# Kernel optimization log

Measured on AMD Instinct MI355X. Metric: run time of the kernel, lower is better.

The kernel has to match this reference:

```python
import jax, jax.numpy as jnp
import numpy as np

N = 2_097_152
EPS = 1e-6


def _tri(x):
    # triangleWave (period 2), maps R -> [0, 1]; applied to 'normalize=True' tables
    return 2.0 * jnp.abs(x / 2.0 - jnp.floor(x / 2.0 + 0.5))


def _grid2d(uv, table, bilinear, normalize):
    # uv: (N,2) in [0,1); table: (U,V,L)
    t = _tri(table) if normalize else table
    U, V, _ = t.shape
    u = jnp.clip(uv[:, 0], 0.0, 1.0 - EPS) * (U - 1)
    v = jnp.clip(uv[:, 1], 0.0, 1.0 - EPS) * (V - 1)
    if bilinear:
        u0 = jnp.floor(u)
        v0 = jnp.floor(v)
        fu = (u - u0)[:, None]
        fv = (v - v0)[:, None]
        u0i = u0.astype(jnp.int32)
        v0i = v0.astype(jnp.int32)
        u1i = jnp.minimum(u0i + 1, U - 1)
        v1i = jnp.minimum(v0i + 1, V - 1)
        return (t[u0i, v0i] * (1 - fu) * (1 - fv)
                + t[u1i, v0i] * fu * (1 - fv)
                + t[u0i, v1i] * (1 - fu) * fv
                + t[u1i, v1i] * fu * fv)
    return t[jnp.round(u).astype(jnp.int32), jnp.round(v).astype(jnp.int32)]


def _grid1d(u, table, bilinear, normalize):
    # u: (N,) in [0,1); table: (U,L)
    t = _tri(table) if normalize else table
    U, _ = t.shape
    uu = jnp.clip(u, 0.0, 1.0 - EPS) * (U - 1)
    if bilinear:
        u0 = jnp.floor(uu)
        fu = (uu - u0)[:, None]
        u0i = u0.astype(jnp.int32)
        u1i = jnp.minimum(u0i + 1, U - 1)
        return t[u0i] * (1 - fu) + t[u1i] * fu
    return t[jnp.round(uu).astype(jnp.int32)]


def setup_inputs() -> dict:
    key = jax.random.key(0)
    ks = jax.random.split(key, 17)
    mk = lambda i, shape: jax.random.uniform(ks[i], shape, dtype=jnp.float32)
    names = ["roughNoh", "anisoToh", "nDotLV", "tDotLV", "metalLoh",
             "subCg", "spst", "shst", "lumCs"]
    d = {n: mk(i, (N, 2)) for i, n in enumerate(names)}
    d["tabRAEnc"] = mk(9, (2048, 2048, 2))
    d["tabCgEnc"] = mk(10, (2048, 1))
    d["tabRSEnc"] = mk(11, (64, 64, 3))
    d["tabRADec"] = mk(12, (48, 48, 3))
    d["tabCgDec"] = mk(13, (96, 2))
    d["tabLVR"] = mk(14, (32, 32, 1))
    d["tabLV"] = mk(15, (32, 32, 4))
    d["tabNHL"] = mk(16, (32, 32, 4))
    return d


def reference(roughNoh, anisoToh, nDotLV, tDotLV, metalLoh, subCg, spst, shst,
              lumCs, tabRAEnc, tabCgEnc, tabRSEnc, tabRADec, tabCgDec,
              tabLVR, tabLV, tabNHL):
    raIn = jnp.stack((roughNoh[:, 0], anisoToh[:, 0]), axis=1)  # (N,2)
    metallicity = metalLoh[:, 0]
    # ---- encoder: LUT lookups + elementwise mixing coefficients ----
    ra = _grid2d(raIn, tabRAEnc, bilinear=False, normalize=True)           # (N,2)
    cg = _grid1d(subCg[:, 1], tabCgEnc, bilinear=False, normalize=True)    # (N,1)
    rsEnc = _grid2d(jnp.concatenate((raIn[:, 0:1], subCg[:, 0:1]), axis=1),
                    tabRSEnc, bilinear=True, normalize=True)               # (N,3)
    cd = (1 - metallicity) * lumCs[:, 0]
    cm0 = (spst[:, 0] * 0.1 * (1 - metallicity) * spst[:, 1]
           + metallicity * lumCs[:, 0])[:, None]
    cm1 = (spst[:, 0] * 0.1 * (1 - metallicity) * (1 - spst[:, 1]))[:, None]
    cs0 = (shst[:, 0] * (1 - metallicity) * shst[:, 1])[:, None]
    cs1 = (shst[:, 0] * (1 - metallicity) * (1 - shst[:, 1]))[:, None]
    cc = (0.25 * 0.25 * lumCs[:, 1])[:, None]
    rsCd = rsEnc * cd[:, None]                                             # (N,3)
    # ---- decoder LUTs ----
    raCoefs = _grid2d(ra, tabRADec, bilinear=True, normalize=False)        # (N,3)
    cgCoefs = _grid1d(cg[:, 0], tabCgDec, bilinear=True, normalize=False)  # (N,2)
    vTerm = _grid2d(jnp.concatenate((nDotLV[:, 0:1] * nDotLV[:, 1:2],
                                     ra[:, 0:1]), axis=1),
                    tabLVR, bilinear=True, normalize=True)                 # (N,1)
    nlvCoefs = _grid2d(nDotLV, tabLV, bilinear=True, normalize=True)       # (N,4)
    nhlCoefs = _grid2d(jnp.stack((metalLoh[:, 1], nDotLV[:, 0]), axis=1),
                       tabNHL, bilinear=True, normalize=True)              # (N,4)
    # ---- elementwise shading combination ----
    noh2 = roughNoh[:, 1] ** 2
    den = raCoefs[:, 0] * anisoToh[:, 1] ** 2 + raCoefs[:, 1] * noh2 + raCoefs[:, 2]
    dTerm = (0.25 / (nDotLV[:, 1] * den ** 2))[:, None]
    x = (rsCd[:, 0:1] * metalLoh[:, 1:2] * nlvCoefs[:, 1:2]
         + rsCd[:, 1:2] * nlvCoefs[:, 2:3]
         + rsCd[:, 2:3] * nlvCoefs[:, 3:4]
         + cm0 * vTerm * nhlCoefs[:, 2:3] * dTerm
         + cs0 * nhlCoefs[:, 0:1])
    y = (((1 - cm1) * nhlCoefs[:, 3:4] + cm1) * vTerm * dTerm
         + cs1 * nhlCoefs[:, 0:1]
         + cc * nhlCoefs[:, 1:2] * nlvCoefs[:, 0:1]
           / (nDotLV[:, 1] * (cgCoefs[:, 0] * noh2 + cgCoefs[:, 1]))[:, None])
    return jnp.concatenate((x, y), axis=1)  # (N,2)
```

## Files before the change

### kernel.cpp

```cpp
#include <hip/hip_runtime.h>
#include <hip/hip_fp16.h>

#define CLIP_HI (1.0f - 1e-6f)

typedef float f4v __attribute__((ext_vector_type(4)));

__device__ __forceinline__ float tri_(float x) {
    return 2.0f * fabsf(x * 0.5f - floorf(x * 0.5f + 0.5f));
}

__device__ __forceinline__ float clamp01(float x) {
    return fminf(fmaxf(x, 0.0f), CLIP_HI);
}

__device__ __forceinline__ float4 nt_load4(const float* p) {
    f4v v = __builtin_nontemporal_load((const f4v*)p);
    return make_float4(v.x, v.y, v.z, v.w);
}
__device__ __forceinline__ void nt_store4(float* p, float4 v) {
    f4v t = {v.x, v.y, v.z, v.w};
    __builtin_nontemporal_store(t, (f4v*)p);
}

struct H4 { __half2 xy, zw; };

struct BW {
    int i00, i10, i01, i11;
    float w00, w10, w01, w11;
};

template <int U, int V>
__device__ __forceinline__ BW bw2d(float uc, float vc) {
    float u = clamp01(uc) * (float)(U - 1);
    float v = clamp01(vc) * (float)(V - 1);
    float u0f = floorf(u), v0f = floorf(v);
    float fu = u - u0f, fv = v - v0f;
    int u0 = (int)u0f, v0 = (int)v0f;
    int u1 = min(u0 + 1, U - 1);
    int v1 = min(v0 + 1, V - 1);
    BW r;
    r.i00 = u0 * V + v0;
    r.i10 = u1 * V + v0;
    r.i01 = u0 * V + v1;
    r.i11 = u1 * V + v1;
    float gu = 1.0f - fu, gv = 1.0f - fv;
    r.w00 = gu * gv; r.w10 = fu * gv; r.w01 = gu * fv; r.w11 = fu * fv;
    return r;
}

__device__ __forceinline__ float4 h4_blend(H4 A, H4 B, H4 C, H4 D, const BW& b) {
    float2 Axy = __half22float2(A.xy), Azw = __half22float2(A.zw);
    float2 Bxy = __half22float2(B.xy), Bzw = __half22float2(B.zw);
    float2 Cxy = __half22float2(C.xy), Czw = __half22float2(C.zw);
    float2 Dxy = __half22float2(D.xy), Dzw = __half22float2(D.zw);
    return make_float4(
        Axy.x * b.w00 + Bxy.x * b.w10 + Cxy.x * b.w01 + Dxy.x * b.w11,
        Axy.y * b.w00 + Bxy.y * b.w10 + Cxy.y * b.w01 + Dxy.y * b.w11,
        Azw.x * b.w00 + Bzw.x * b.w10 + Czw.x * b.w01 + Dzw.x * b.w11,
        Azw.y * b.w00 + Bzw.y * b.w10 + Czw.y * b.w01 + Dzw.y * b.w11);
}

__global__ __launch_bounds__(256) void prep_rs_kernel(const float* __restrict__ t,
                                                      H4* __restrict__ o) {
    int j = blockIdx.x * 256 + threadIdx.x;
    if (j < 64 * 64) {
        float a = tri_(t[j * 3 + 0]);
        float b = tri_(t[j * 3 + 1]);
        float c = tri_(t[j * 3 + 2]);
        H4 h;
        h.xy = __floats2half2_rn(a, b);
        h.zw = __floats2half2_rn(c, 0.0f);
        o[j] = h;
    }
}

__device__ __forceinline__ float2 gatherRA(const float* __restrict__ tabRAEnc,
                                           float rNx, float aTx) {
    int ui = (int)rintf(clamp01(rNx) * 2047.0f);
    int vi = (int)rintf(clamp01(aTx) * 2047.0f);
    return ((const float2*)tabRAEnc)[ui * 2048 + vi];
}

template <bool USE_WS>
__device__ __forceinline__ float2 shadeB(
    float rNx, float rNy, float aTy, float nLVx, float nLVy,
    float mLx, float mLy, float sCx, float sCy, float spx, float spy,
    float shx, float shy, float lCx, float lCy,
    float2 raT,
    const float* __restrict__ tabRSEnc, const H4* __restrict__ rsPacked,
    const H4* sRADec, const __half2* sCgComp, const __half* sLVR,
    const H4* sLV, const H4* sNHL)
{
    float rs0, rs1, rs2;
    {
        BW b = bw2d<64, 64>(rNx, sCx);
        if constexpr (USE_WS) {
            float4 r = h4_blend(rsPacked[b.i00], rsPacked[b.i10],
                                rsPacked[b.i01], rsPacked[b.i11], b);
            rs0 = r.x; rs1 = r.y; rs2 = r.z;
        } else {
            const float* p00 = tabRSEnc + b.i00 * 3;
            const float* p10 = tabRSEnc + b.i10 * 3;
            const float* p01 = tabRSEnc + b.i01 * 3;
            const float* p11 = tabRSEnc + b.i11 * 3;
            rs0 = tri_(p00[0]) * b.w00 + tri_(p10[0]) * b.w10 + tri_(p01[0]) * b.w01 + tri_(p11[0]) * b.w11;
            rs1 = tri_(p00[1]) * b.w00 + tri_(p10[1]) * b.w10 + tri_(p01[1]) * b.w01 + tri_(p11[1]) * b.w11;
            rs2 = tri_(p00[2]) * b.w00 + tri_(p10[2]) * b.w10 + tri_(p01[2]) * b.w01 + tri_(p11[2]) * b.w11;
        }
    }

    float2 cgC = __half22float2(sCgComp[(int)rintf(clamp01(sCy) * 2047.0f)]);

    float4 nlv, nhl;
    {
        BW b = bw2d<32, 32>(nLVx, nLVy);
        nlv = h4_blend(sLV[b.i00], sLV[b.i10], sLV[b.i01], sLV[b.i11], b);
    }
    {
        BW b = bw2d<32, 32>(mLy, nLVx);
        nhl = h4_blend(sNHL[b.i00], sNHL[b.i10], sNHL[b.i01], sNHL[b.i11], b);
    }

    float ra0 = tri_(raT.x);
    float ra1 = tri_(raT.y);

    float raC0, raC1, raC2;
    {
        BW b = bw2d<48, 48>(ra0, ra1);
        float4 r = h4_blend(sRADec[b.i00], sRADec[b.i10],
                            sRADec[b.i01], sRADec[b.i11], b);
        raC0 = r.x; raC1 = r.y; raC2 = r.z;
    }

    float vTerm;
    {
        BW b = bw2d<32, 32>(nLVx * nLVy, ra0);
        vTerm = __half2float(sLVR[b.i00]) * b.w00 + __half2float(sLVR[b.i10]) * b.w10 +
                __half2float(sLVR[b.i01]) * b.w01 + __half2float(sLVR[b.i11]) * b.w11;
    }

    float met = mLx;
    float om  = 1.0f - met;
    float cd  = om * lCx;
    float cm0 = spx * 0.1f * om * spy + met * lCx;
    float cm1 = spx * 0.1f * om * (1.0f - spy);
    float cs0 = shx * om * shy;
    float cs1 = shx * om * (1.0f - shy);
    float cc  = 0.0625f * lCy;

    float noh2 = rNy * rNy;
    float den  = raC0 * aTy * aTy + raC1 * noh2 + raC2;
    float dTerm = 0.25f / (nLVy * den * den);

    float x = rs0 * cd * mLy * nlv.y + rs1 * cd * nlv.z + rs2 * cd * nlv.w
            + cm0 * vTerm * nhl.z * dTerm + cs0 * nhl.x;

    float y = ((1.0f - cm1) * nhl.w + cm1) * vTerm * dTerm
            + cs1 * nhl.x
            + cc * nhl.y * nlv.x / (nLVy * (cgC.x * noh2 + cgC.y));

    return make_float2(x, y);
}

template <bool USE_WS>
__global__ __launch_bounds__(512, 6) void disney_main(
    const float* __restrict__ roughNoh,
    const float* __restrict__ anisoToh,
    const float* __restrict__ nDotLV,
    const float* __restrict__ metalLoh,
    const float* __restrict__ subCg,
    const float* __restrict__ spst,
    const float* __restrict__ shst,
    const float* __restrict__ lumCs,
    const float* __restrict__ tabRAEnc,
    const float* __restrict__ tabCgEnc,
    const float* __restrict__ tabRSEnc,
    const H4*    __restrict__ rsPacked,
    const float* __restrict__ tabRADec,
    const float* __restrict__ tabCgDec,
    const float* __restrict__ tabLVR,
    const float* __restrict__ tabLV,
    const float* __restrict__ tabNHL,
    float* __restrict__ out,
    int n)
{
    __shared__ H4      sRADec[48 * 48];
    __shared__ __half2 sCgComp[2048];
    __shared__ __half  sLVR[1024];
    __shared__ H4      sLV[1024];
    __shared__ H4      sNHL[1024];

    int tid = threadIdx.x;

    for (int j = tid; j < 48 * 48; j += 512) {
        H4 h;
        h.xy = __floats2half2_rn(tabRADec[j * 3 + 0], tabRADec[j * 3 + 1]);
        h.zw = __floats2half2_rn(tabRADec[j * 3 + 2], 0.0f);
        sRADec[j] = h;
    }
#pragma unroll
    for (int k = 0; k < 4; ++k) {
        int j = tid + k * 512;
        float cg = tri_(tabCgEnc[j]);
        float u = clamp01(cg) * 95.0f;
        float u0f = floorf(u);
        float fu = u - u0f;
        int u0 = (int)u0f;
        int u1 = min(u0 + 1, 95);
        float2 a = ((const float2*)tabCgDec)[u0];
        float2 b = ((const float2*)tabCgDec)[u1];
        sCgComp[j] = __floats2half2_rn(a.x * (1.0f - fu) + b.x * fu,
                                       a.y * (1.0f - fu) + b.y * fu);
    }
#pragma unroll
    for (int k = 0; k < 2; ++k) {
        int j = tid + k * 512;
        sLVR[j] = __float2half(tri_(tabLVR[j]));
        float4 v = ((const float4*)tabLV)[j];
        H4 h; h.xy = __floats2half2_rn(tri_(v.x), tri_(v.y));
              h.zw = __floats2half2_rn(tri_(v.z), tri_(v.w));
        sLV[j] = h;
        float4 w = ((const float4*)tabNHL)[j];
        H4 h2; h2.xy = __floats2half2_rn(tri_(w.x), tri_(w.y));
               h2.zw = __floats2half2_rn(tri_(w.z), tri_(w.w));
        sNHL[j] = h2;
    }
    __syncthreads();

    int P = (n + 1) >> 1;
    int H = (P + 1) >> 1;
    int t = blockIdx.x * 512 + tid;
    if (t >= H) return;
    int p1 = t;
    int p2 = t + H;

    bool full1 = (2 * p1 + 1) < n;
    bool full2 = (p2 < P) && ((2 * p2 + 1) < n);

    if (full1 && full2) {
        float4 rN1 = nt_load4(roughNoh + 4 * p1);
        float4 aT1 = nt_load4(anisoToh + 4 * p1);
        float4 rN2 = nt_load4(roughNoh + 4 * p2);
        float4 aT2 = nt_load4(anisoToh + 4 * p2);

        float2 raT0 = gatherRA(tabRAEnc, rN1.x, aT1.x);
        float2 raT1 = gatherRA(tabRAEnc, rN1.z, aT1.z);
        float2 raT2 = gatherRA(tabRAEnc, rN2.x, aT2.x);
        float2 raT3 = gatherRA(tabRAEnc, rN2.z, aT2.z);

        float4 nLV1 = nt_load4(nDotLV   + 4 * p1);
        float4 mL1  = nt_load4(metalLoh + 4 * p1);
        float4 sC1  = nt_load4(subCg    + 4 * p1);
        float4 sp1  = nt_load4(spst     + 4 * p1);
        float4 sh1  = nt_load4(shst     + 4 * p1);
        float4 lC1  = nt_load4(lumCs    + 4 * p1);
        float4 nLV2 = nt_load4(nDotLV   + 4 * p2);
        float4 mL2  = nt_load4(metalLoh + 4 * p2);
        float4 sC2  = nt_load4(subCg    + 4 * p2);
        float4 sp2  = nt_load4(spst     + 4 * p2);
        float4 sh2  = nt_load4(shst     + 4 * p2);
        float4 lC2  = nt_load4(lumCs    + 4 * p2);

        float2 r0 = shadeB<USE_WS>(rN1.x, rN1.y, aT1.y, nLV1.x, nLV1.y,
                                   mL1.x, mL1.y, sC1.x, sC1.y, sp1.x, sp1.y,
                                   sh1.x, sh1.y, lC1.x, lC1.y, raT0,
                                   tabRSEnc, rsPacked,
                                   sRADec, sCgComp, sLVR, sLV, sNHL);
        float2 r1 = shadeB<USE_WS>(rN1.z, rN1.w, aT1.w, nLV1.z, nLV1.w,
                                   mL1.z, mL1.w, sC1.z, sC1.w, sp1.z, sp1.w,
                                   sh1.z, sh1.w, lC1.z, lC1.w, raT1,
                                   tabRSEnc, rsPacked,
                                   sRADec, sCgComp, sLVR, sLV, sNHL);
        nt_store4(out + 4 * p1, make_float4(r0.x, r0.y, r1.x, r1.y));

        float2 r2 = shadeB<USE_WS>(rN2.x, rN2.y, aT2.y, nLV2.x, nLV2.y,
                                   mL2.x, mL2.y, sC2.x, sC2.y, sp2.x, sp2.y,
                                   sh2.x, sh2.y, lC2.x, lC2.y, raT2,
                                   tabRSEnc, rsPacked,
                                   sRADec, sCgComp, sLVR, sLV, sNHL);
        float2 r3 = shadeB<USE_WS>(rN2.z, rN2.w, aT2.w, nLV2.z, nLV2.w,
                                   mL2.z, mL2.w, sC2.z, sC2.w, sp2.z, sp2.w,
                                   sh2.z, sh2.w, lC2.z, lC2.w, raT3,
                                   tabRSEnc, rsPacked,
                                   sRADec, sCgComp, sLVR, sLV, sNHL);
        nt_store4(out + 4 * p2, make_float4(r2.x, r2.y, r3.x, r3.y));
    } else {
        int es[4] = { 2 * p1, 2 * p1 + 1,
                      (p2 < P) ? 2 * p2 : n, (p2 < P) ? 2 * p2 + 1 : n };
#pragma unroll
        for (int k = 0; k < 4; ++k) {
            int e = es[k];
            if (e >= n) continue;
            float2 rN  = ((const float2*)roughNoh)[e];
            float2 aT  = ((const float2*)anisoToh)[e];
            float2 nLV = ((const float2*)nDotLV)[e];
            float2 mL  = ((const float2*)metalLoh)[e];
            float2 sC  = ((const float2*)subCg)[e];
            float2 sp  = ((const float2*)spst)[e];
            float2 sh  = ((const float2*)shst)[e];
            float2 lC  = ((const float2*)lumCs)[e];
            float2 raT = gatherRA(tabRAEnc, rN.x, aT.x);
            float2 r = shadeB<USE_WS>(rN.x, rN.y, aT.y, nLV.x, nLV.y,
                                      mL.x, mL.y, sC.x, sC.y, sp.x, sp.y,
                                      sh.x, sh.y, lC.x, lC.y, raT,
                                      tabRSEnc, rsPacked,
                                      sRADec, sCgComp, sLVR, sLV, sNHL);
            ((float2*)out)[e] = r;
        }
    }
}

extern "C" void kernel_launch(void* const* d_in, const int* in_sizes, int n_in,
                              void* d_out, int out_size, void* d_ws, size_t ws_size,
                              hipStream_t stream) {
    const float* roughNoh = (const float*)d_in[0];
    const float* anisoToh = (const float*)d_in[1];
    const float* nDotLV   = (const float*)d_in[2];
    const float* metalLoh = (const float*)d_in[4];
    const float* subCg    = (const float*)d_in[5];
    const float* spst     = (const float*)d_in[6];
    const float* shst     = (const float*)d_in[7];
    const float* lumCs    = (const float*)d_in[8];
    const float* tabRAEnc = (const float*)d_in[9];
    const float* tabCgEnc = (const float*)d_in[10];
    const float* tabRSEnc = (const float*)d_in[11];
    const float* tabRADec = (const float*)d_in[12];
    const float* tabCgDec = (const float*)d_in[13];
    const float* tabLVR   = (const float*)d_in[14];
    const float* tabLV    = (const float*)d_in[15];
    const float* tabNHL   = (const float*)d_in[16];

    int n = in_sizes[0] / 2;
    float* out = (float*)d_out;

    const int block = 512;
    int P = (n + 1) / 2;
    int H = (P + 1) / 2;
    int grid = (H + block - 1) / block;

    bool use_ws = ws_size >= (size_t)(64 * 64 * sizeof(H4));
    if (use_ws) {
        prep_rs_kernel<<<(64 * 64 + 255) / 256, 256, 0, stream>>>(tabRSEnc, (H4*)d_ws);
        disney_main<true><<<grid, block, 0, stream>>>(
            roughNoh, anisoToh, nDotLV, metalLoh, subCg, spst, shst, lumCs,
            tabRAEnc, tabCgEnc, tabRSEnc, (const H4*)d_ws,
            tabRADec, tabCgDec, tabLVR, tabLV, tabNHL, out, n);
    } else {
        disney_main<false><<<grid, block, 0, stream>>>(
            roughNoh, anisoToh, nDotLV, metalLoh, subCg, spst, shst, lumCs,
            tabRAEnc, tabCgEnc, tabRSEnc, (const H4*)d_ws,
            tabRADec, tabCgDec, tabLVR, tabLV, tabNHL, out, n);
    }
}
```

Baseline: 235.8 us.

## Split random RA-encoder table gather into a separate pre-pass kernel

Adds a ra_pass kernel that gathers from the 32MB tabRAEnc table and applies the triangle wave, writing per-element results to a workspace buffer. The main shading kernel then streams these values in coalesced form instead of doing the random gathers inline. The aim is to separate latency-bound random gathers from the compute- and LDS-heavy main kernel so each can reach higher occupancy. The cost is an extra 16MB write plus re-read and re-reading the two input arrays; the path needs enough workspace, otherwise it falls back to the old path.

```diff
diff --git a/kernel.cpp b/kernel.cpp
--- a/kernel.cpp
+++ b/kernel.cpp
@@ -22,7 +22,7 @@
     __builtin_nontemporal_store(t, (f4v*)p);
 }
 
-struct H4 { __half2 xy, zw; };
+struct __attribute__((aligned(8))) H4 { __half2 xy, zw; };
 
 struct BW {
     int i00, i10, i01, i11;
@@ -81,12 +81,62 @@
     return ((const float2*)tabRAEnc)[ui * 2048 + vi];
 }
 
+__global__ __launch_bounds__(512, 8) void ra_pass(
+    const float* __restrict__ roughNoh,
+    const float* __restrict__ anisoToh,
+    const float* __restrict__ tabRAEnc,
+    float2* __restrict__ raBuf,
+    int n)
+{
+    int P = n >> 1;
+    int Q = P >> 2;
+    int t = blockIdx.x * 512 + threadIdx.x;
+    if (t < Q) {
+        int p0 = t, p1 = t + Q, p2 = t + 2 * Q, p3 = t + 3 * Q;
+        float4 a0 = nt_load4(roughNoh + 4 * p0);
+        float4 b0 = nt_load4(anisoToh + 4 * p0);
+        float4 a1 = nt_load4(roughNoh + 4 * p1);
+        float4 b1 = nt_load4(anisoToh + 4 * p1);
+        float4 a2 = nt_load4(roughNoh + 4 * p2);
+        float4 b2 = nt_load4(anisoToh + 4 * p2);
+        float4 a3 = nt_load4(roughNoh + 4 * p3);
+        float4 b3 = nt_load4(anisoToh + 4 * p3);
+
+        float2 g0 = gatherRA(tabRAEnc, a0.x, b0.x);
+        float2 g1 = gatherRA(tabRAEnc, a0.z, b0.z);
+        float2 g2 = gatherRA(tabRAEnc, a1.x, b1.x);
+        float2 g3 = gatherRA(tabRAEnc, a1.z, b1.z);
+        float2 g4 = gatherRA(tabRAEnc, a2.x, b2.x);
+        float2 g5 = gatherRA(tabRAEnc, a2.z, b2.z);
+        float2 g6 = gatherRA(tabRAEnc, a3.x, b3.x);
+        float2 g7 = gatherRA(tabRAEnc, a3.z, b3.z);
+
+        nt_store4((float*)(raBuf + 2 * p0),
+                  make_float4(tri_(g0.x), tri_(g0.y), tri_(g1.x), tri_(g1.y)));
+        nt_store4((float*)(raBuf + 2 * p1),
+                  make_float4(tri_(g2.x), tri_(g2.y), tri_(g3.x), tri_(g3.y)));
+        nt_store4((float*)(raBuf + 2 * p2),
+                  make_float4(tri_(g4.x), tri_(g4.y), tri_(g5.x), tri_(g5.y)));
+        nt_store4((float*)(raBuf + 2 * p3),
+                  make_float4(tri_(g6.x), tri_(g6.y), tri_(g7.x), tri_(g7.y)));
+    }
+    int tail = 8 * Q;
+    int rem = n - tail;
+    if (blockIdx.x == 0 && threadIdx.x < rem) {
+        int e = tail + threadIdx.x;
+        float2 rN = ((const float2*)roughNoh)[e];
+        float2 aT = ((const float2*)anisoToh)[e];
+        float2 g = gatherRA(tabRAEnc, rN.x, aT.x);
+        raBuf[e] = make_float2(tri_(g.x), tri_(g.y));
+    }
+}
+
 template <bool USE_WS>
 __device__ __forceinline__ float2 shadeB(
     float rNx, float rNy, float aTy, float nLVx, float nLVy,
     float mLx, float mLy, float sCx, float sCy, float spx, float spy,
     float shx, float shy, float lCx, float lCy,
-    float2 raT,
+    float ra0, float ra1,
     const float* __restrict__ tabRSEnc, const H4* __restrict__ rsPacked,
     const H4* sRADec, const __half2* sCgComp, const __half* sLVR,
     const H4* sLV, const H4* sNHL)
@@ -121,9 +171,6 @@
         nhl = h4_blend(sNHL[b.i00], sNHL[b.i10], sNHL[b.i01], sNHL[b.i11], b);
     }
 
-    float ra0 = tri_(raT.x);
-    float ra1 = tri_(raT.y);
-
     float raC0, raC1, raC2;
     {
         BW b = bw2d<48, 48>(ra0, ra1);
@@ -162,7 +209,7 @@
     return make_float2(x, y);
 }
 
-template <bool USE_WS>
+template <bool USE_WS, bool RA_WS>
 __global__ __launch_bounds__(512, 6) void disney_main(
     const float* __restrict__ roughNoh,
     const float* __restrict__ anisoToh,
@@ -173,6 +220,7 @@
     const float* __restrict__ shst,
     const float* __restrict__ lumCs,
     const float* __restrict__ tabRAEnc,
+    const float2* __restrict__ raBuf,
     const float* __restrict__ tabCgEnc,
     const float* __restrict__ tabRSEnc,
     const H4*    __restrict__ rsPacked,
@@ -243,10 +291,18 @@
         float4 rN2 = nt_load4(roughNoh + 4 * p2);
         float4 aT2 = nt_load4(anisoToh + 4 * p2);
 
-        float2 raT0 = gatherRA(tabRAEnc, rN1.x, aT1.x);
-        float2 raT1 = gatherRA(tabRAEnc, rN1.z, aT1.z);
-        float2 raT2 = gatherRA(tabRAEnc, rN2.x, aT2.x);
-        float2 raT3 = gatherRA(tabRAEnc, rN2.z, aT2.z);
+        float4 raA, raB;
+        if constexpr (RA_WS) {
+            raA = nt_load4((const float*)(raBuf + 2 * p1));
+            raB = nt_load4((const float*)(raBuf + 2 * p2));
+        } else {
+            float2 g0 = gatherRA(tabRAEnc, rN1.x, aT1.x);
+            float2 g1 = gatherRA(tabRAEnc, rN1.z, aT1.z);
+            float2 g2 = gatherRA(tabRAEnc, rN2.x, aT2.x);
+            float2 g3 = gatherRA(tabRAEnc, rN2.z, aT2.z);
+            raA = make_float4(tri_(g0.x), tri_(g0.y), tri_(g1.x), tri_(g1.y));
+            raB = make_float4(tri_(g2.x), tri_(g2.y), tri_(g3.x), tri_(g3.y));
+        }
 
         float4 nLV1 = nt_load4(nDotLV   + 4 * p1);
         float4 mL1  = nt_load4(metalLoh + 4 * p1);
@@ -263,24 +319,24 @@
 
         float2 r0 = shadeB<USE_WS>(rN1.x, rN1.y, aT1.y, nLV1.x, nLV1.y,
                                    mL1.x, mL1.y, sC1.x, sC1.y, sp1.x, sp1.y,
-                                   sh1.x, sh1.y, lC1.x, lC1.y, raT0,
+                                   sh1.x, sh1.y, lC1.x, lC1.y, raA.x, raA.y,
                                    tabRSEnc, rsPacked,
                                    sRADec, sCgComp, sLVR, sLV, sNHL);
         float2 r1 = shadeB<USE_WS>(rN1.z, rN1.w, aT1.w, nLV1.z, nLV1.w,
                                    mL1.z, mL1.w, sC1.z, sC1.w, sp1.z, sp1.w,
-                                   sh1.z, sh1.w, lC1.z, lC1.w, raT1,
+                                   sh1.z, sh1.w, lC1.z, lC1.w, raA.z, raA.w,
                                    tabRSEnc, rsPacked,
                                    sRADec, sCgComp, sLVR, sLV, sNHL);
         nt_store4(out + 4 * p1, make_float4(r0.x, r0.y, r1.x, r1.y));
 
         float2 r2 = shadeB<USE_WS>(rN2.x, rN2.y, aT2.y, nLV2.x, nLV2.y,
                                    mL2.x, mL2.y, sC2.x, sC2.y, sp2.x, sp2.y,
-                                   sh2.x, sh2.y, lC2.x, lC2.y, raT2,
+                                   sh2.x, sh2.y, lC2.x, lC2.y, raB.x, raB.y,
                                    tabRSEnc, rsPacked,
                                    sRADec, sCgComp, sLVR, sLV, sNHL);
         float2 r3 = shadeB<USE_WS>(rN2.z, rN2.w, aT2.w, nLV2.z, nLV2.w,
                                    mL2.z, mL2.w, sC2.z, sC2.w, sp2.z, sp2.w,
-                                   sh2.z, sh2.w, lC2.z, lC2.w, raT3,
+                                   sh2.z, sh2.w, lC2.z, lC2.w, raB.z, raB.w,
                                    tabRSEnc, rsPacked,
                                    sRADec, sCgComp, sLVR, sLV, sNHL);
         nt_store4(out + 4 * p2, make_float4(r2.x, r2.y, r3.x, r3.y));
@@ -299,10 +355,17 @@
             float2 sp  = ((const float2*)spst)[e];
             float2 sh  = ((const float2*)shst)[e];
             float2 lC  = ((const float2*)lumCs)[e];
-            float2 raT = gatherRA(tabRAEnc, rN.x, aT.x);
+            float ra0, ra1;
+            if constexpr (RA_WS) {
+                float2 g = raBuf[e];
+                ra0 = g.x; ra1 = g.y;
+            } else {
+                float2 g = gatherRA(tabRAEnc, rN.x, aT.x);
+                ra0 = tri_(g.x); ra1 = tri_(g.y);
+            }
             float2 r = shadeB<USE_WS>(rN.x, rN.y, aT.y, nLV.x, nLV.y,
                                       mL.x, mL.y, sC.x, sC.y, sp.x, sp.y,
-                                      sh.x, sh.y, lC.x, lC.y, raT,
+                                      sh.x, sh.y, lC.x, lC.y, ra0, ra1,
                                       tabRSEnc, rsPacked,
                                       sRADec, sCgComp, sLVR, sLV, sNHL);
             ((float2*)out)[e] = r;
@@ -336,19 +399,29 @@
     const int block = 512;
     int P = (n + 1) / 2;
     int H = (P + 1) / 2;
-    int grid = (H + block - 1) / block;
-
-    bool use_ws = ws_size >= (size_t)(64 * 64 * sizeof(H4));
-    if (use_ws) {
-        prep_rs_kernel<<<(64 * 64 + 255) / 256, 256, 0, stream>>>(tabRSEnc, (H4*)d_ws);
-        disney_main<true><<<grid, block, 0, stream>>>(
+    int grid_main = (H + block - 1) / block;
+
+    size_t need = 32768 + (size_t)n * sizeof(float2);
+
+    if (ws_size >= need) {
+        H4*     rsPacked = (H4*)d_ws;
+        float2* raBuf    = (float2*)((char*)d_ws + 32768);
+
+        prep_rs_kernel<<<(64 * 64 + 255) / 256, 256, 0, stream>>>(tabRSEnc, rsPacked);
+
+        int Q = (n >> 1) >> 2;
+        int grid_ra = (Q + block - 1) / block;
+        if (grid_ra < 1) grid_ra = 1;
+        ra_pass<<<grid_ra, block, 0, stream>>>(roughNoh, anisoToh, tabRAEnc, raBuf, n);
+
+        disney_main<true, true><<<grid_main, block, 0, stream>>>(
             roughNoh, anisoToh, nDotLV, metalLoh, subCg, spst, shst, lumCs,
-            tabRAEnc, tabCgEnc, tabRSEnc, (const H4*)d_ws,
+            tabRAEnc, raBuf, tabCgEnc, tabRSEnc, rsPacked,
             tabRADec, tabCgDec, tabLVR, tabLV, tabNHL, out, n);
     } else {
-        disney_main<false><<<grid, block, 0, stream>>>(
+        disney_main<false, false><<<grid_main, block, 0, stream>>>(
             roughNoh, anisoToh, nDotLV, metalLoh, subCg, spst, shst, lumCs,
-            tabRAEnc, tabCgEnc, tabRSEnc, (const H4*)d_ws,
+            tabRAEnc, (const float2*)d_ws, tabCgEnc, tabRSEnc, (const H4*)d_ws,
             tabRADec, tabCgDec, tabLVR, tabLV, tabNHL, out, n);
     }
 }
```

After: 263.0 us. +11.5%, slower.
